# Optimization experiments

Hardware: AMD Instinct MI355X
Metric: run time of the kernel (lower is better)

Reference implementation:

```python
import jax, jax.numpy as jnp
import numpy as np

NEG_INF = -1e9  # matches the TF additive-mask constant


def setup_inputs() -> dict:
    key = jax.random.key(0)
    k1, k2, k3 = jax.random.split(key, 3)
    B, Tq, Tk, D = 8, 2048, 2048, 1024
    decoder_outputs = jax.random.normal(k1, (B, Tq, D), dtype=jnp.float32)
    encoder_outputs = jax.random.normal(k2, (B, Tk, D), dtype=jnp.float32)
    encoder_mask = jax.random.randint(k3, (B, Tk), 0, 2, dtype=jnp.int32)
    return {
        "decoder_outputs": decoder_outputs,
        "encoder_outputs": encoder_outputs,
        "encoder_mask": encoder_mask,
    }


def reference(decoder_outputs, encoder_outputs, encoder_mask):
    # score[b, q, k] = <dec[b, q], enc[b, k]>  (no 1/sqrt(d) scaling in original)
    score = jnp.einsum("bqd,bkd->bqk", decoder_outputs, encoder_outputs)
    m = encoder_mask.astype(score.dtype)[:, None, :]  # [B, 1, Tk]
    score = score + (1.0 - m) * NEG_INF
    attention_weights = jax.nn.softmax(score, axis=-1)
    context_vector = jnp.einsum("bqk,bkd->bqd", attention_weights, encoder_outputs)
    return (context_vector, attention_weights)
```

## Files before the change

kernel.cpp:

```cpp
#include <hip/hip_runtime.h>
#include <cstddef>
#include <cstdint>

typedef _Float16 f16x8 __attribute__((ext_vector_type(8)));
typedef _Float16 f16x4 __attribute__((ext_vector_type(4)));
typedef float f32x4 __attribute__((ext_vector_type(4)));

static constexpr int BATCH = 8;
static constexpr int TQ = 2048;
static constexpr int TK = 2048;
static constexpr int DIM = 1024;
static constexpr size_t CTX_ELEMS = (size_t)BATCH * TQ * DIM;
static constexpr size_t ATT_ELEMS = (size_t)BATCH * TQ * TK;

static constexpr size_t WS_DEC = 0;
static constexpr size_t WS_ENC = WS_DEC + CTX_ELEMS;
static constexpr size_t WS_ENCT = WS_ENC + CTX_ELEMS;
static constexpr size_t WS_W = WS_ENCT + CTX_ELEMS;
static constexpr size_t WS_NEEDED_BYTES = (WS_W + ATT_ELEMS) * 2;

__device__ __forceinline__ void async16(const void* g, const void* l) {
  __builtin_amdgcn_global_load_lds(
      (const __attribute__((address_space(1))) unsigned int*)g,
      (__attribute__((address_space(3))) unsigned int*)l, 16, 0, 0);
}

__device__ __forceinline__ f16x8 cvt8(float4 a, float4 b) {
  f16x8 h;
  h[0] = (_Float16)a.x; h[1] = (_Float16)a.y; h[2] = (_Float16)a.z; h[3] = (_Float16)a.w;
  h[4] = (_Float16)b.x; h[5] = (_Float16)b.y; h[6] = (_Float16)b.z; h[7] = (_Float16)b.w;
  return h;
}


__global__ __launch_bounds__(256) void convert_kernel(
    const float* __restrict__ enc, const float* __restrict__ dec,
    _Float16* __restrict__ enc16, _Float16* __restrict__ encT,
    _Float16* __restrict__ dec16) {
  __shared__ _Float16 sT[64 * 72];
  const int k0 = blockIdx.x * 64, d0 = blockIdx.y * 64, b = blockIdx.z;
  const int t = threadIdx.x;
  const int krow = t >> 2;
  const int dcol = (t & 3) * 16;

  const float* src = enc + ((size_t)b * TK + k0 + krow) * DIM + d0 + dcol;
  float4 f0 = *(const float4*)(src);
  float4 f1 = *(const float4*)(src + 4);
  float4 f2 = *(const float4*)(src + 8);
  float4 f3 = *(const float4*)(src + 12);
  _Float16 h[16];
#pragma unroll
  for (int i = 0; i < 4; i++) {
    h[i]      = (_Float16)((&f0.x)[i]);
    h[i + 4]  = (_Float16)((&f1.x)[i]);
    h[i + 8]  = (_Float16)((&f2.x)[i]);
    h[i + 12] = (_Float16)((&f3.x)[i]);
  }
  _Float16* dsts = enc16 + ((size_t)b * TK + k0 + krow) * DIM + d0 + dcol;
  *(f16x8*)dsts = *(const f16x8*)&h[0];
  *(f16x8*)(dsts + 8) = *(const f16x8*)&h[8];
#pragma unroll
  for (int i = 0; i < 16; i++)
    sT[(dcol + i) * 72 + krow] = h[i];

  {
    const int bid = ((blockIdx.z * gridDim.y) + blockIdx.y) * gridDim.x + blockIdx.x;
    size_t base = (size_t)bid * 4096 + (size_t)t * 16;
    float4 a0 = *(const float4*)(dec + base);
    float4 a1 = *(const float4*)(dec + base + 4);
    float4 a2 = *(const float4*)(dec + base + 8);
    float4 a3 = *(const float4*)(dec + base + 12);
    *(f16x8*)(dec16 + base) = cvt8(a0, a1);
    *(f16x8*)(dec16 + base + 8) = cvt8(a2, a3);
  }

  __syncthreads();

  const int drow = t >> 2;
  const int kg = (t & 3) * 16;
  f16x8 v0 = *(const f16x8*)&sT[drow * 72 + kg];
  f16x8 v1 = *(const f16x8*)&sT[drow * 72 + kg + 8];
  _Float16* dst = encT + ((size_t)b * DIM + d0 + drow) * TK + k0 + kg;
  *(f16x8*)dst = v0;
  *(f16x8*)(dst + 8) = v1;
}


template <int KD>
__device__ __forceinline__ void stage_sub(const _Float16* __restrict__ Xb,
                                          _Float16* slot, int khalf,
                                          int w, int srow, int schunk) {
#pragma unroll
  for (int j = 0; j < 2; ++j) {
    const int row0 = 16 * (j * 8 + w);
    async16(Xb + (size_t)(row0 + srow) * KD + khalf + schunk * 8,
            slot + row0 * 32);
  }
}

__device__ __forceinline__ void load4s(f16x8 (&dst)[4], const _Float16* base) {
#pragma unroll
  for (int i = 0; i < 4; ++i) dst[i] = *(const f16x8*)(base + i * 512);
}

__device__ __forceinline__ void mfma16(f32x4 (&acc)[8][4], const f16x8 (&aF)[4],
                                       const f16x8 (&bF)[4], int mh) {
  __builtin_amdgcn_s_setprio(1);
#pragma unroll
  for (int i = 0; i < 4; ++i)
#pragma unroll
    for (int j = 0; j < 4; ++j)
      acc[mh * 4 + i][j] = __builtin_amdgcn_mfma_f32_16x16x32_f16(
          aF[i], bF[j], acc[mh * 4 + i][j], 0, 0, 0);
  __builtin_amdgcn_s_setprio(0);
}

template <int M, int N, int K>
__global__ __launch_bounds__(512, 2) void gemm8p(
    const _Float16* __restrict__ A, const _Float16* __restrict__ B,
    float* __restrict__ C) {
  __shared__ _Float16 lds[65536];
  constexpr int T = K / 64;

  const int b = blockIdx.x, nt = blockIdx.y, mt = blockIdx.z;
  const int tid = threadIdx.x;
  const int lane = tid & 63, w = tid >> 6;
  const int tm = lane & 15, quad = lane >> 4;
  const int wr = w >> 2, wc = w & 3;

  const _Float16* Ab = A + ((size_t)b * M + mt * 256) * K;
  const _Float16* Bb = B + ((size_t)b * N + nt * 256) * K;

  const int srow = lane >> 2;
  const int schunk = (lane & 3) ^ (srow & 3);

  const int xorc = (quad ^ (tm & 3)) * 8;
  const int aBase = (wr * 128 + tm) * 32 + xorc;
  const int bBase = (wc * 64 + tm) * 32 + xorc;

  f32x4 acc[8][4] = {};

  stage_sub<K>(Ab, lds, 0, w, srow, schunk);
  stage_sub<K>(Bb, lds + 32768, 0, w, srow, schunk);
  stage_sub<K>(Ab, lds + 16384, 32, w, srow, schunk);
  stage_sub<K>(Bb, lds + 49152, 32, w, srow, schunk);
  stage_sub<K>(Ab, lds + 8192, 64, w, srow, schunk);
  stage_sub<K>(Bb, lds + 32768 + 8192, 64, w, srow, schunk);
  asm volatile("s_waitcnt vmcnt(8)" ::: "memory");
  __builtin_amdgcn_s_barrier();

  for (int t = 0; t < T; ++t) {
    const int p = t & 1, np = p ^ 1;
    _Float16* const aLo = lds + p * 8192;
    _Float16* const aHi = lds + 16384 + p * 8192;
    _Float16* const bLo = lds + 32768 + p * 8192;
    _Float16* const bHi = lds + 49152 + p * 8192;
    const bool s1 = (t + 1 < T), s2 = (t + 2 < T);
    f16x8 aF[4], bF[4];

    load4s(aF, aLo + aBase);
    load4s(bF, bLo + bBase);
    if (s1) stage_sub<K>(Ab, lds + 16384 + np * 8192, (t + 1) * 64 + 32, w, srow, schunk);
    __builtin_amdgcn_s_barrier();
    mfma16(acc, aF, bF, 0);
    __builtin_amdgcn_s_barrier();

    load4s(aF, aLo + aBase + 2048);
    if (s1) {
      stage_sub<K>(Bb, lds + 49152 + np * 8192, (t + 1) * 64 + 32, w, srow, schunk);
      asm volatile("s_waitcnt vmcnt(8)" ::: "memory");
    } else {
      asm volatile("s_waitcnt vmcnt(0)" ::: "memory");
    }
    __builtin_amdgcn_s_barrier();
    mfma16(acc, aF, bF, 1);
    __builtin_amdgcn_s_barrier();

    load4s(aF, aHi + aBase);
    load4s(bF, bHi + bBase);
    if (s2) stage_sub<K>(Ab, lds + p * 8192, (t + 2) * 64, w, srow, schunk);
    __builtin_amdgcn_s_barrier();
    mfma16(acc, aF, bF, 0);
    __builtin_amdgcn_s_barrier();

    load4s(aF, aHi + aBase + 2048);
    if (s2) {
      stage_sub<K>(Bb, lds + 32768 + p * 8192, (t + 2) * 64, w, srow, schunk);
      asm volatile("s_waitcnt vmcnt(8)" ::: "memory");
    } else if (t + 2 == T) {
      asm volatile("s_waitcnt vmcnt(4)" ::: "memory");
    }
    __builtin_amdgcn_s_barrier();
    mfma16(acc, aF, bF, 1);
    __builtin_amdgcn_s_barrier();
  }

#pragma unroll
  for (int i = 0; i < 8; ++i) {
#pragma unroll
    for (int rr = 0; rr < 4; ++rr) {
      size_t row = (size_t)b * M + mt * 256 + wr * 128 + i * 16 + quad * 4 + rr;
      float* Crow = C + row * (size_t)N + nt * 256 + wc * 64 + tm;
#pragma unroll
      for (int j = 0; j < 4; ++j) Crow[j * 16] = acc[i][j][rr];
    }
  }
}

__global__ __launch_bounds__(256) void softmax_kernel(
    float* __restrict__ S, const int* __restrict__ mask, _Float16* __restrict__ W16) {
  const int row = blockIdx.x;
  const int b = row >> 11;
  float* srow = S + (size_t)row * TK;
  const int* mrow = mask + (size_t)b * TK;
  const int t = threadIdx.x;

  float4 s0 = *(const float4*)(srow + t * 8);
  float4 s1 = *(const float4*)(srow + t * 8 + 4);
  int4 m0 = *(const int4*)(mrow + t * 8);
  int4 m1 = *(const int4*)(mrow + t * 8 + 4);

  float v[8] = {s0.x, s0.y, s0.z, s0.w, s1.x, s1.y, s1.z, s1.w};
  const int mm[8] = {m0.x, m0.y, m0.z, m0.w, m1.x, m1.y, m1.z, m1.w};
#pragma unroll
  for (int i = 0; i < 8; i++)
    if (!mm[i]) v[i] += -1e9f;

  float mx = v[0];
#pragma unroll
  for (int i = 1; i < 8; i++) mx = fmaxf(mx, v[i]);
#pragma unroll
  for (int off = 32; off > 0; off >>= 1) mx = fmaxf(mx, __shfl_down(mx, off));

  __shared__ float redm[4];
  __shared__ float reds[4];
  if ((t & 63) == 0) redm[t >> 6] = mx;
  __syncthreads();
  mx = fmaxf(fmaxf(redm[0], redm[1]), fmaxf(redm[2], redm[3]));

  float e[8];
  float lsum = 0.f;
#pragma unroll
  for (int i = 0; i < 8; i++) {
    e[i] = __expf(v[i] - mx);
    lsum += e[i];
  }
#pragma unroll
  for (int off = 32; off > 0; off >>= 1) lsum += __shfl_down(lsum, off);
  if ((t & 63) == 0) reds[t >> 6] = lsum;
  __syncthreads();
  const float inv = 1.0f / (reds[0] + reds[1] + reds[2] + reds[3]);

  float4 o0 = {e[0] * inv, e[1] * inv, e[2] * inv, e[3] * inv};
  float4 o1 = {e[4] * inv, e[5] * inv, e[6] * inv, e[7] * inv};
  *(float4*)(srow + t * 8) = o0;
  *(float4*)(srow + t * 8 + 4) = o1;
  if (W16) {
    f16x8 h;
    h[0] = (_Float16)o0.x; h[1] = (_Float16)o0.y; h[2] = (_Float16)o0.z; h[3] = (_Float16)o0.w;
    h[4] = (_Float16)o1.x; h[5] = (_Float16)o1.y; h[6] = (_Float16)o1.z; h[7] = (_Float16)o1.w;
    *(f16x8*)(W16 + (size_t)row * TK + t * 8) = h;
  }
}

static constexpr int BM = 128, BN = 128, BK = 32;
static constexpr int LDSS = 40;

__global__ __launch_bounds__(256) void score_kernel_fb(
    const float* __restrict__ dec, const float* __restrict__ enc,
    float* __restrict__ S) {
  __shared__ _Float16 sA[BM * LDSS];
  __shared__ _Float16 sB[BN * LDSS];
  const int nt = blockIdx.x, mt = blockIdx.y, b = blockIdx.z;
  const int t = threadIdx.x;
  const int lane = t & 63, wave = t >> 6;
  const int wm = wave >> 1, wn = wave & 1;
  const int tm = lane & 15, quad = lane >> 4;
  const float* Abase = dec + ((size_t)b * TQ + mt * BM) * DIM;
  const float* Bbase = enc + ((size_t)b * TK + nt * BN) * DIM;
  f32x4 acc[4][4] = {};
  const int r = t >> 2;
  const int c8 = (t & 3) * 8;
  for (int k0 = 0; k0 < DIM; k0 += BK) {
    float4 a0 = *(const float4*)(Abase + (size_t)r * DIM + k0 + c8);
    float4 a1 = *(const float4*)(Abase + (size_t)r * DIM + k0 + c8 + 4);
    float4 a2 = *(const float4*)(Abase + (size_t)(r + 64) * DIM + k0 + c8);
    float4 a3 = *(const float4*)(Abase + (size_t)(r + 64) * DIM + k0 + c8 + 4);
    float4 b0 = *(const float4*)(Bbase + (size_t)r * DIM + k0 + c8);
    float4 b1 = *(const float4*)(Bbase + (size_t)r * DIM + k0 + c8 + 4);
    float4 b2 = *(const float4*)(Bbase + (size_t)(r + 64) * DIM + k0 + c8);
    float4 b3 = *(const float4*)(Bbase + (size_t)(r + 64) * DIM + k0 + c8 + 4);
    __syncthreads();
    *(f16x8*)&sA[r * LDSS + c8] = cvt8(a0, a1);
    *(f16x8*)&sA[(r + 64) * LDSS + c8] = cvt8(a2, a3);
    *(f16x8*)&sB[r * LDSS + c8] = cvt8(b0, b1);
    *(f16x8*)&sB[(r + 64) * LDSS + c8] = cvt8(b2, b3);
    __syncthreads();
    f16x8 aF[4], bF[4];
#pragma unroll
    for (int i = 0; i < 4; i++)
      aF[i] = *(const f16x8*)&sA[(wm * 64 + i * 16 + tm) * LDSS + quad * 8];
#pragma unroll
    for (int j = 0; j < 4; j++)
      bF[j] = *(const f16x8*)&sB[(wn * 64 + j * 16 + tm) * LDSS + quad * 8];
#pragma unroll
    for (int i = 0; i < 4; i++)
#pragma unroll
      for (int j = 0; j < 4; j++)
        acc[i][j] = __builtin_amdgcn_mfma_f32_16x16x32_f16(aF[i], bF[j], acc[i][j], 0, 0, 0);
  }
#pragma unroll
  for (int i = 0; i < 4; i++) {
#pragma unroll
    for (int rr = 0; rr < 4; rr++) {
      size_t rowoff = ((size_t)b * TQ + mt * BM + wm * 64 + i * 16 + quad * 4 + rr) * (size_t)TK;
#pragma unroll
      for (int j = 0; j < 4; j++)
        S[rowoff + nt * BN + wn * 64 + j * 16 + tm] = acc[i][j][rr];
    }
  }
}

__global__ __launch_bounds__(256) void ctx_kernel_fb(
    const float* __restrict__ W, const float* __restrict__ enc,
    float* __restrict__ C) {
  __shared__ _Float16 sA[BM * LDSS];
  __shared__ _Float16 sB[BN * LDSS];
  const int nt = blockIdx.x;
  const int mt = blockIdx.y;
  const int b = blockIdx.z;
  const int t = threadIdx.x;
  const int lane = t & 63, wave = t >> 6;
  const int wm = wave >> 1, wn = wave & 1;
  const int tm = lane & 15, quad = lane >> 4;
  const float* Abase = W + ((size_t)b * TQ + mt * BM) * TK;
  const float* Ebase = enc + (size_t)b * TK * DIM + nt * BN;
  f32x4 acc[4][4] = {};
  const int r = t >> 2;
  const int c8 = (t & 3) * 8;
  const int kkB = (t & 7) * 4;
  const int nnB = (t >> 3) * 4;
  for (int k0 = 0; k0 < TK; k0 += BK) {
    float4 a0 = *(const float4*)(Abase + (size_t)r * TK + k0 + c8);
    float4 a1 = *(const float4*)(Abase + (size_t)r * TK + k0 + c8 + 4);
    float4 a2 = *(const float4*)(Abase + (size_t)(r + 64) * TK + k0 + c8);
    float4 a3 = *(const float4*)(Abase + (size_t)(r + 64) * TK + k0 + c8 + 4);
    float4 f[4];
#pragma unroll
    for (int i = 0; i < 4; i++)
      f[i] = *(const float4*)(Ebase + (size_t)(k0 + kkB + i) * DIM + nnB);
    __syncthreads();
    *(f16x8*)&sA[r * LDSS + c8] = cvt8(a0, a1);
    *(f16x8*)&sA[(r + 64) * LDSS + c8] = cvt8(a2, a3);
#pragma unroll
    for (int c = 0; c < 4; c++) {
      f16x4 h;
      h[0] = (_Float16)((&f[0].x)[c]);
      h[1] = (_Float16)((&f[1].x)[c]);
      h[2] = (_Float16)((&f[2].x)[c]);
      h[3] = (_Float16)((&f[3].x)[c]);
      *(f16x4*)&sB[(nnB + c) * LDSS + kkB] = h;
    }
    __syncthreads();
    f16x8 aF[4], bF[4];
#pragma unroll
    for (int i = 0; i < 4; i++)
      aF[i] = *(const f16x8*)&sA[(wm * 64 + i * 16 + tm) * LDSS + quad * 8];
#pragma unroll
    for (int j = 0; j < 4; j++)
      bF[j] = *(const f16x8*)&sB[(wn * 64 + j * 16 + tm) * LDSS + quad * 8];
#pragma unroll
    for (int i = 0; i < 4; i++)
#pragma unroll
      for (int j = 0; j < 4; j++)
        acc[i][j] = __builtin_amdgcn_mfma_f32_16x16x32_f16(aF[i], bF[j], acc[i][j], 0, 0, 0);
  }
#pragma unroll
  for (int i = 0; i < 4; i++) {
#pragma unroll
    for (int rr = 0; rr < 4; rr++) {
      size_t rowoff = ((size_t)b * TQ + mt * BM + wm * 64 + i * 16 + quad * 4 + rr) * (size_t)DIM;
#pragma unroll
      for (int j = 0; j < 4; j++)
        C[rowoff + nt * BN + wn * 64 + j * 16 + tm] = acc[i][j][rr];
    }
  }
}

extern "C" void kernel_launch(void* const* d_in, const int* in_sizes, int n_in,
                              void* d_out, int out_size, void* d_ws, size_t ws_size,
                              hipStream_t stream) {
  const float* dec = (const float*)d_in[0];
  const float* enc = (const float*)d_in[1];
  const int* mask = (const int*)d_in[2];

  float* ctx = (float*)d_out;
  float* attn = (float*)d_out + CTX_ELEMS;

  dim3 block(256);

  if (ws_size >= WS_NEEDED_BYTES) {
    _Float16* dec16 = (_Float16*)d_ws + WS_DEC;
    _Float16* enc16 = (_Float16*)d_ws + WS_ENC;
    _Float16* encT = (_Float16*)d_ws + WS_ENCT;
    _Float16* W16 = (_Float16*)d_ws + WS_W;

    convert_kernel<<<dim3(TK / 64, DIM / 64, BATCH), block, 0, stream>>>(
        enc, dec, enc16, encT, dec16);
    gemm8p<TQ, TK, DIM><<<dim3(BATCH, TK / 256, TQ / 256), dim3(512), 0, stream>>>(dec16, enc16, attn);
    softmax_kernel<<<dim3(BATCH * TQ), block, 0, stream>>>(attn, mask, W16);
    gemm8p<TQ, DIM, TK><<<dim3(BATCH, DIM / 256, TQ / 256), dim3(512), 0, stream>>>(W16, encT, ctx);
  } else {
    score_kernel_fb<<<dim3(TK / BN, TQ / BM, BATCH), block, 0, stream>>>(dec, enc, attn);
    softmax_kernel<<<dim3(BATCH * TQ), block, 0, stream>>>(attn, mask, nullptr);
    ctx_kernel_fb<<<dim3(DIM / BN, TQ / BM, BATCH), block, 0, stream>>>(attn, enc, ctx);
  }
}
```

Before: 486.0 us.

## Fuse score GEMM with masked softmax and convert decoder inside kernel

Replaces the separate decoder conversion, score GEMM and softmax kernels with one kernel. Each 512-thread block holds a 32-row strip of decoder (converted to fp16 in LDS) against the full 2048-key row, and computes the scores with MFMA. Mask, max, exp and sum run in registers with a cross-wave LDS reduction, then fp32 attention and fp16 weights are written once. This drops the fp32 score round trip through HBM and the dec16 buffer. The cost is that encoder fragments are read straight from global memory without LDS staging, heavy register use (128 accumulators per thread), and a grid of only 512 blocks.

```diff
diff --git a/kernel.cpp b/kernel.cpp
--- a/kernel.cpp
+++ b/kernel.cpp
@@ -13,8 +13,7 @@
 static constexpr size_t CTX_ELEMS = (size_t)BATCH * TQ * DIM;
 static constexpr size_t ATT_ELEMS = (size_t)BATCH * TQ * TK;
 
-static constexpr size_t WS_DEC = 0;
-static constexpr size_t WS_ENC = WS_DEC + CTX_ELEMS;
+static constexpr size_t WS_ENC = 0;
 static constexpr size_t WS_ENCT = WS_ENC + CTX_ELEMS;
 static constexpr size_t WS_W = WS_ENCT + CTX_ELEMS;
 static constexpr size_t WS_NEEDED_BYTES = (WS_W + ATT_ELEMS) * 2;
@@ -33,10 +32,9 @@
 }
 
 
-__global__ __launch_bounds__(256) void convert_kernel(
-    const float* __restrict__ enc, const float* __restrict__ dec,
-    _Float16* __restrict__ enc16, _Float16* __restrict__ encT,
-    _Float16* __restrict__ dec16) {
+__global__ __launch_bounds__(256) void convert_enc_kernel(
+    const float* __restrict__ enc, _Float16* __restrict__ enc16,
+    _Float16* __restrict__ encT) {
   __shared__ _Float16 sT[64 * 72];
   const int k0 = blockIdx.x * 64, d0 = blockIdx.y * 64, b = blockIdx.z;
   const int t = threadIdx.x;
@@ -62,18 +60,6 @@
 #pragma unroll
   for (int i = 0; i < 16; i++)
     sT[(dcol + i) * 72 + krow] = h[i];
-
-  {
-    const int bid = ((blockIdx.z * gridDim.y) + blockIdx.y) * gridDim.x + blockIdx.x;
-    size_t base = (size_t)bid * 4096 + (size_t)t * 16;
-    float4 a0 = *(const float4*)(dec + base);
-    float4 a1 = *(const float4*)(dec + base + 4);
-    float4 a2 = *(const float4*)(dec + base + 8);
-    float4 a3 = *(const float4*)(dec + base + 12);
-    *(f16x8*)(dec16 + base) = cvt8(a0, a1);
-    *(f16x8*)(dec16 + base + 8) = cvt8(a2, a3);
-  }
-
   __syncthreads();
 
   const int drow = t >> 2;
@@ -85,6 +71,153 @@
   *(f16x8*)(dst + 8) = v1;
 }
 
+__global__ __launch_bounds__(512, 2) void score_softmax_kernel(
+    const float* __restrict__ dec, const _Float16* __restrict__ enc16,
+    const int* __restrict__ mask, float* __restrict__ attn,
+    _Float16* __restrict__ W16) {
+  __shared__ _Float16 sA[32 * 1024];
+  __shared__ float red[2][32][8];
+
+  const int fid = blockIdx.y * 64 + blockIdx.x;
+  const int b = fid & 7;
+  const int mt = fid >> 3;
+  const int tid = threadIdx.x;
+  const int lane = tid & 63, w = tid >> 6;
+  const int tm = lane & 15, quad = lane >> 4;
+
+  const float* Ab = dec + ((size_t)b * TQ + mt * 32) * DIM;
+  const _Float16* Bb = enc16 + (size_t)b * TK * DIM;
+  const int n0 = w * 256;
+
+#pragma unroll
+  for (int k = 0; k < 8; ++k) {
+    const int c = tid + 512 * k;
+    const int row = c >> 7, cc = c & 127;
+    const float* g = Ab + (size_t)row * DIM + cc * 8;
+    float4 f0 = *(const float4*)g;
+    float4 f1 = *(const float4*)(g + 4);
+    *(f16x8*)&sA[(size_t)(row * 128 + (cc ^ (row & 7))) * 8] = cvt8(f0, f1);
+  }
+  __syncthreads();
+
+  f32x4 acc[2][16] = {};
+  for (int ks = 0; ks < 32; ++ks) {
+    f16x8 bF[16];
+    const _Float16* bp = Bb + (size_t)(n0 + tm) * DIM + ks * 32 + quad * 8;
+#pragma unroll
+    for (int j = 0; j < 16; ++j)
+      bF[j] = *(const f16x8*)(bp + (size_t)(j * 16) * DIM);
+    f16x8 aF[2];
+#pragma unroll
+    for (int Mt = 0; Mt < 2; ++Mt) {
+      const int r = Mt * 16 + tm;
+      const int cc = (ks * 4 + quad) ^ (r & 7);
+      aF[Mt] = *(const f16x8*)&sA[(size_t)(r * 128 + cc) * 8];
+    }
+    __builtin_amdgcn_s_setprio(1);
+#pragma unroll
+    for (int Mt = 0; Mt < 2; ++Mt)
+#pragma unroll
+      for (int j = 0; j < 16; ++j)
+        acc[Mt][j] = __builtin_amdgcn_mfma_f32_16x16x32_f16(
+            aF[Mt], bF[j], acc[Mt][j], 0, 0, 0);
+    __builtin_amdgcn_s_setprio(0);
+  }
+
+  float mk[16];
+  const int* mrow = mask + (size_t)b * TK + n0 + tm;
+#pragma unroll
+  for (int j = 0; j < 16; ++j) mk[j] = mrow[j * 16] ? 0.f : -1e9f;
+#pragma unroll
+  for (int Mt = 0; Mt < 2; ++Mt)
+#pragma unroll
+    for (int j = 0; j < 16; ++j)
+#pragma unroll
+      for (int rr = 0; rr < 4; ++rr)
+        acc[Mt][j][rr] += mk[j];
+
+  float rmax[2][4];
+#pragma unroll
+  for (int Mt = 0; Mt < 2; ++Mt)
+#pragma unroll
+    for (int rr = 0; rr < 4; ++rr) {
+      float m = acc[Mt][0][rr];
+#pragma unroll
+      for (int j = 1; j < 16; ++j) m = fmaxf(m, acc[Mt][j][rr]);
+#pragma unroll
+      for (int off = 1; off < 16; off <<= 1) m = fmaxf(m, __shfl_xor(m, off));
+      rmax[Mt][rr] = m;
+    }
+  if (tm == 0) {
+#pragma unroll
+    for (int Mt = 0; Mt < 2; ++Mt)
+#pragma unroll
+      for (int rr = 0; rr < 4; ++rr)
+        red[0][Mt * 16 + quad * 4 + rr][w] = rmax[Mt][rr];
+  }
+  __syncthreads();
+#pragma unroll
+  for (int Mt = 0; Mt < 2; ++Mt)
+#pragma unroll
+    for (int rr = 0; rr < 4; ++rr) {
+      const float* rp = red[0][Mt * 16 + quad * 4 + rr];
+      float m = rp[0];
+#pragma unroll
+      for (int i = 1; i < 8; ++i) m = fmaxf(m, rp[i]);
+      rmax[Mt][rr] = m;
+    }
+
+  float rsum[2][4];
+#pragma unroll
+  for (int Mt = 0; Mt < 2; ++Mt)
+#pragma unroll
+    for (int rr = 0; rr < 4; ++rr) {
+      float s = 0.f;
+#pragma unroll
+      for (int j = 0; j < 16; ++j) {
+        float e = __expf(acc[Mt][j][rr] - rmax[Mt][rr]);
+        acc[Mt][j][rr] = e;
+        s += e;
+      }
+#pragma unroll
+      for (int off = 1; off < 16; off <<= 1) s += __shfl_xor(s, off);
+      rsum[Mt][rr] = s;
+    }
+  if (tm == 0) {
+#pragma unroll
+    for (int Mt = 0; Mt < 2; ++Mt)
+#pragma unroll
+      for (int rr = 0; rr < 4; ++rr)
+        red[1][Mt * 16 + quad * 4 + rr][w] = rsum[Mt][rr];
+  }
+  __syncthreads();
+#pragma unroll
+  for (int Mt = 0; Mt < 2; ++Mt)
+#pragma unroll
+    for (int rr = 0; rr < 4; ++rr) {
+      const float* rp = red[1][Mt * 16 + quad * 4 + rr];
+      float s = rp[0];
+#pragma unroll
+      for (int i = 1; i < 8; ++i) s += rp[i];
+      rsum[Mt][rr] = s;
+    }
+
+#pragma unroll
+  for (int Mt = 0; Mt < 2; ++Mt)
+#pragma unroll
+    for (int rr = 0; rr < 4; ++rr) {
+      const float inv = 1.0f / rsum[Mt][rr];
+      const size_t grow = (size_t)b * TQ + mt * 32 + Mt * 16 + quad * 4 + rr;
+      float* ap = attn + grow * (size_t)TK + n0 + tm;
+      _Float16* wp = W16 + grow * (size_t)TK + n0 + tm;
+#pragma unroll
+      for (int j = 0; j < 16; ++j) {
+        float o = acc[Mt][j][rr] * inv;
+        ap[j * 16] = o;
+        wp[j * 16] = (_Float16)o;
+      }
+    }
+}
 
 template <int KD>
 __device__ __forceinline__ void stage_sub(const _Float16* __restrict__ Xb,
@@ -400,15 +533,12 @@
   dim3 block(256);
 
   if (ws_size >= WS_NEEDED_BYTES) {
-    _Float16* dec16 = (_Float16*)d_ws + WS_DEC;
     _Float16* enc16 = (_Float16*)d_ws + WS_ENC;
     _Float16* encT = (_Float16*)d_ws + WS_ENCT;
     _Float16* W16 = (_Float16*)d_ws + WS_W;
 
-    convert_kernel<<<dim3(TK / 64, DIM / 64, BATCH), block, 0, stream>>>(
-        enc, dec, enc16, encT, dec16);
-    gemm8p<TQ, TK, DIM><<<dim3(BATCH, TK / 256, TQ / 256), dim3(512), 0, stream>>>(dec16, enc16, attn);
-    softmax_kernel<<<dim3(BATCH * TQ), block, 0, stream>>>(attn, mask, W16);
+    convert_enc_kernel<<<dim3(TK / 64, DIM / 64, BATCH), block, 0, stream>>>(enc, enc16, encT);
+    score_softmax_kernel<<<dim3(64, 8), dim3(512), 0, stream>>>(dec, enc16, mask, attn, W16);
     gemm8p<TQ, DIM, TK><<<dim3(BATCH, DIM / 256, TQ / 256), dim3(512), 0, stream>>>(W16, encT, ctx);
   } else {
     score_kernel_fb<<<dim3(TK / BN, TQ / BM, BATCH), block, 0, stream>>>(dec, enc, attn);
```

After: 604.5 us. +24.4%, slower.

## Restructure fp16 GEMM staging into 64-wide half-tiles with simpler double buffering

Applied to the files above, without the earlier changes.

Replaces the staggered four-stage 32-wide K-half staging in both GEMMs with a double-buffered layout of four 128x64 half-tiles per stage, swizzled with an 8-way XOR. All next-stage loads are issued at the top of each iteration and drained with a single vmcnt(0) at its end. This aims to cut barrier and waitcnt bookkeeping, make wider 128-byte row loads, and reduce LDS bank conflicts. The cost is less fine-grained overlap, since each iteration must wait for its whole next-stage prefetch before continuing.

```diff
diff --git a/kernel.cpp b/kernel.cpp
--- a/kernel.cpp
+++ b/kernel.cpp
@@ -85,38 +85,21 @@
   *(f16x8*)(dst + 8) = v1;
 }
 
+static constexpr int HT = 8192;
 
 template <int KD>
-__device__ __forceinline__ void stage_sub(const _Float16* __restrict__ Xb,
-                                          _Float16* slot, int khalf,
-                                          int w, int srow, int schunk) {
+__device__ __forceinline__ void stage_ht(const _Float16* __restrict__ Xb,
+                                         _Float16* ht, int khalf, int w, int lane) {
 #pragma unroll
   for (int j = 0; j < 2; ++j) {
-    const int row0 = 16 * (j * 8 + w);
-    async16(Xb + (size_t)(row0 + srow) * KD + khalf + schunk * 8,
-            slot + row0 * 32);
-  }
-}
-
-__device__ __forceinline__ void load4s(f16x8 (&dst)[4], const _Float16* base) {
-#pragma unroll
-  for (int i = 0; i < 4; ++i) dst[i] = *(const f16x8*)(base + i * 512);
-}
-
-__device__ __forceinline__ void mfma16(f32x4 (&acc)[8][4], const f16x8 (&aF)[4],
-                                       const f16x8 (&bF)[4], int mh) {
-  __builtin_amdgcn_s_setprio(1);
-#pragma unroll
-  for (int i = 0; i < 4; ++i)
-#pragma unroll
-    for (int j = 0; j < 4; ++j)
-      acc[mh * 4 + i][j] = __builtin_amdgcn_mfma_f32_16x16x32_f16(
-          aF[i], bF[j], acc[mh * 4 + i][j], 0, 0, 0);
-  __builtin_amdgcn_s_setprio(0);
+    const int r = w * 16 + j * 8 + (lane >> 3);
+    const int slot = (lane & 7) ^ (r & 7);
+    async16(Xb + (size_t)r * KD + khalf + slot * 8, ht + (w * 16 + j * 8) * 64);
+  }
 }
 
 template <int M, int N, int K>
-__global__ __launch_bounds__(512, 2) void gemm8p(
+__global__ __launch_bounds__(512, 2) void gemm_cf(
     const _Float16* __restrict__ A, const _Float16* __restrict__ B,
     float* __restrict__ C) {
   __shared__ _Float16 lds[65536];
@@ -130,68 +113,92 @@
 
   const _Float16* Ab = A + ((size_t)b * M + mt * 256) * K;
   const _Float16* Bb = B + ((size_t)b * N + nt * 256) * K;
-
-  const int srow = lane >> 2;
-  const int schunk = (lane & 3) ^ (srow & 3);
-
-  const int xorc = (quad ^ (tm & 3)) * 8;
-  const int aBase = (wr * 128 + tm) * 32 + xorc;
-  const int bBase = (wc * 64 + tm) * 32 + xorc;
+  const _Float16* src[4] = {Ab, Ab + (size_t)128 * K, Bb, Bb + (size_t)128 * K};
+
+  const int aht = wr;
+  const int bht = 2 + (wc >> 1);
+  const int brow = (wc & 1) * 64;
+
+  const int s0 = (quad ^ (tm & 7)) * 8;
+  const int s1 = s0 ^ 32;
 
   f32x4 acc[8][4] = {};
 
-  stage_sub<K>(Ab, lds, 0, w, srow, schunk);
-  stage_sub<K>(Bb, lds + 32768, 0, w, srow, schunk);
-  stage_sub<K>(Ab, lds + 16384, 32, w, srow, schunk);
-  stage_sub<K>(Bb, lds + 49152, 32, w, srow, schunk);
-  stage_sub<K>(Ab, lds + 8192, 64, w, srow, schunk);
-  stage_sub<K>(Bb, lds + 32768 + 8192, 64, w, srow, schunk);
-  asm volatile("s_waitcnt vmcnt(8)" ::: "memory");
+#pragma unroll
+  for (int q = 0; q < 4; ++q)
+    stage_ht<K>(src[q], lds + q * HT, 0, w, lane);
+  asm volatile("s_waitcnt vmcnt(0)" ::: "memory");
   __builtin_amdgcn_s_barrier();
 
   for (int t = 0; t < T; ++t) {
     const int p = t & 1, np = p ^ 1;
-    _Float16* const aLo = lds + p * 8192;
-    _Float16* const aHi = lds + 16384 + p * 8192;
-    _Float16* const bLo = lds + 32768 + p * 8192;
-    _Float16* const bHi = lds + 49152 + p * 8192;
-    const bool s1 = (t + 1 < T), s2 = (t + 2 < T);
+    const _Float16* hA = lds + (p * 4 + aht) * HT;
+    const _Float16* hB = lds + (p * 4 + bht) * HT;
     f16x8 aF[4], bF[4];
 
-    load4s(aF, aLo + aBase);
-    load4s(bF, bLo + bBase);
-    if (s1) stage_sub<K>(Ab, lds + 16384 + np * 8192, (t + 1) * 64 + 32, w, srow, schunk);
-    __builtin_amdgcn_s_barrier();
-    mfma16(acc, aF, bF, 0);
-    __builtin_amdgcn_s_barrier();
-
-    load4s(aF, aLo + aBase + 2048);
-    if (s1) {
-      stage_sub<K>(Bb, lds + 49152 + np * 8192, (t + 1) * 64 + 32, w, srow, schunk);
-      asm volatile("s_waitcnt vmcnt(8)" ::: "memory");
-    } else {
-      asm volatile("s_waitcnt vmcnt(0)" ::: "memory");
+#pragma unroll
+    for (int j = 0; j < 4; ++j)
+      bF[j] = *(const f16x8*)(hB + (brow + j * 16 + tm) * 64 + s0);
+#pragma unroll
+    for (int i = 0; i < 4; ++i)
+      aF[i] = *(const f16x8*)(hA + (i * 16 + tm) * 64 + s0);
+    if (t + 1 < T) {
+      const int kh = (t + 1) * 64;
+#pragma unroll
+      for (int q = 0; q < 4; ++q)
+        stage_ht<K>(src[q], lds + (np * 4 + q) * HT, kh, w, lane);
     }
     __builtin_amdgcn_s_barrier();
-    mfma16(acc, aF, bF, 1);
-    __builtin_amdgcn_s_barrier();
-
-    load4s(aF, aHi + aBase);
-    load4s(bF, bHi + bBase);
-    if (s2) stage_sub<K>(Ab, lds + p * 8192, (t + 2) * 64, w, srow, schunk);
-    __builtin_amdgcn_s_barrier();
-    mfma16(acc, aF, bF, 0);
-    __builtin_amdgcn_s_barrier();
-
-    load4s(aF, aHi + aBase + 2048);
-    if (s2) {
-      stage_sub<K>(Bb, lds + 32768 + p * 8192, (t + 2) * 64, w, srow, schunk);
-      asm volatile("s_waitcnt vmcnt(8)" ::: "memory");
-    } else if (t + 2 == T) {
-      asm volatile("s_waitcnt vmcnt(4)" ::: "memory");
-    }
-    __builtin_amdgcn_s_barrier();
-    mfma16(acc, aF, bF, 1);
+    __builtin_amdgcn_s_setprio(1);
+#pragma unroll
+    for (int i = 0; i < 4; ++i)
+#pragma unroll
+      for (int j = 0; j < 4; ++j)
+        acc[i][j] = __builtin_amdgcn_mfma_f32_16x16x32_f16(aF[i], bF[j], acc[i][j], 0, 0, 0);
+    __builtin_amdgcn_s_setprio(0);
+    __builtin_amdgcn_s_barrier();
+
+#pragma unroll
+    for (int i = 0; i < 4; ++i)
+      aF[i] = *(const f16x8*)(hA + (64 + i * 16 + tm) * 64 + s0);
+    __builtin_amdgcn_s_barrier();
+    __builtin_amdgcn_s_setprio(1);
+#pragma unroll
+    for (int i = 0; i < 4; ++i)
+#pragma unroll
+      for (int j = 0; j < 4; ++j)
+        acc[4 + i][j] = __builtin_amdgcn_mfma_f32_16x16x32_f16(aF[i], bF[j], acc[4 + i][j], 0, 0, 0);
+    __builtin_amdgcn_s_setprio(0);
+    __builtin_amdgcn_s_barrier();
+
+#pragma unroll
+    for (int j = 0; j < 4; ++j)
+      bF[j] = *(const f16x8*)(hB + (brow + j * 16 + tm) * 64 + s1);
+#pragma unroll
+    for (int i = 0; i < 4; ++i)
+      aF[i] = *(const f16x8*)(hA + (i * 16 + tm) * 64 + s1);
+    __builtin_amdgcn_s_barrier();
+    __builtin_amdgcn_s_setprio(1);
+#pragma unroll
+    for (int i = 0; i < 4; ++i)
+#pragma unroll
+      for (int j = 0; j < 4; ++j)
+        acc[i][j] = __builtin_amdgcn_mfma_f32_16x16x32_f16(aF[i], bF[j], acc[i][j], 0, 0, 0);
+    __builtin_amdgcn_s_setprio(0);
+    __builtin_amdgcn_s_barrier();
+
+#pragma unroll
+    for (int i = 0; i < 4; ++i)
+      aF[i] = *(const f16x8*)(hA + (64 + i * 16 + tm) * 64 + s1);
+    __builtin_amdgcn_s_barrier();
+    __builtin_amdgcn_s_setprio(1);
+#pragma unroll
+    for (int i = 0; i < 4; ++i)
+#pragma unroll
+      for (int j = 0; j < 4; ++j)
+        acc[4 + i][j] = __builtin_amdgcn_mfma_f32_16x16x32_f16(aF[i], bF[j], acc[4 + i][j], 0, 0, 0);
+    __builtin_amdgcn_s_setprio(0);
+    asm volatile("s_waitcnt vmcnt(0)" ::: "memory");
     __builtin_amdgcn_s_barrier();
   }
 
@@ -407,9 +414,9 @@
 
     convert_kernel<<<dim3(TK / 64, DIM / 64, BATCH), block, 0, stream>>>(
         enc, dec, enc16, encT, dec16);
-    gemm8p<TQ, TK, DIM><<<dim3(BATCH, TK / 256, TQ / 256), dim3(512), 0, stream>>>(dec16, enc16, attn);
+    gemm_cf<TQ, TK, DIM><<<dim3(BATCH, TK / 256, TQ / 256), dim3(512), 0, stream>>>(dec16, enc16, attn);
     softmax_kernel<<<dim3(BATCH * TQ), block, 0, stream>>>(attn, mask, W16);
-    gemm8p<TQ, DIM, TK><<<dim3(BATCH, DIM / 256, TQ / 256), dim3(512), 0, stream>>>(W16, encT, ctx);
+    gemm_cf<TQ, DIM, TK><<<dim3(BATCH, DIM / 256, TQ / 256), dim3(512), 0, stream>>>(W16, encT, ctx);
   } else {
     score_kernel_fb<<<dim3(TK / BN, TQ / BM, BATCH), block, 0, stream>>>(dec, enc, attn);
     softmax_kernel<<<dim3(BATCH * TQ), block, 0, stream>>>(attn, mask, nullptr);
```

After: 489.1 us. No clear change (+0.6%).
